# Kernel tuning notes

Measured on AMD Instinct MI355X. Metric: run time of the kernel, lower is better.

## Reference

```python
import jax, jax.numpy as jnp
import numpy as np
from jax import lax

B, P, D = 4, 8192, 512          # 4 point clouds, 8192 pts each, 512-dim features
SCALES = (1.0, 0.5, 0.25)
BIG = 1e10


def fps_indices(pos_b, n_samples):
    """Farthest-point sampling on one cloud. pos_b: [P,3] -> idx [n_samples].
    Deterministic start at index 0 (original uses a random start)."""
    n_pts = pos_b.shape[0]

    def step(carry, _):
        dist, far = carry                       # dist:[P], far: scalar int
        centroid = pos_b[far]                   # [3]
        d = jnp.sum((pos_b - centroid) ** 2, axis=-1)  # [P]
        dist = jnp.minimum(dist, d)
        new_far = jnp.argmax(dist).astype(jnp.int32)
        return (dist, new_far), far

    init = (jnp.full((n_pts,), BIG, dtype=pos_b.dtype), jnp.int32(0))
    _, idx = lax.scan(step, init, None, length=n_samples)
    return idx                                  # [n_samples] int32


def setup_inputs() -> dict:
    key = jax.random.key(0)
    k1, k2 = jax.random.split(key)
    x = jax.random.normal(k1, (B * P, D), dtype=jnp.float32)
    pos = jax.random.normal(k2, (B * P, 3), dtype=jnp.float32)
    batch_idx = jnp.repeat(jnp.arange(B, dtype=jnp.int64), P)  # sorted, equal-sized batches
    return {"x": x, "pos": pos, "batch_idx": batch_idx}


def reference(x, pos, batch_idx):
    # batch_idx is sorted with equal counts -> per-batch view is a reshape
    xb = x.reshape(B, P, D)
    pb = pos.reshape(B, P, 3)

    feats = [xb]          # scale == 1.0 keeps all points
    poss = [pb]
    for s in SCALES[1:]:
        n = max(1, int(P * s))
        idx = jax.vmap(lambda p: fps_indices(p, n))(pb)          # [B, n]
        feats.append(jnp.take_along_axis(xb, idx[:, :, None], axis=1))  # [B, n, D]
        poss.append(jnp.take_along_axis(pb, idx[:, :, None], axis=1))   # [B, n, 3]

    # 'concat' fusion: per-batch concat over scales, then concat over batches
    fused_x = jnp.concatenate(feats, axis=1).reshape(-1, D)
    fused_p = jnp.concatenate(poss, axis=1).reshape(-1, 3)
    return fused_x, fused_p
```

## Files before the change

### kernel.cpp

```cpp
#include <hip/hip_runtime.h>


constexpr int kB   = 4;
constexpr int kP   = 8192;
constexpr int kD   = 512;
constexpr int kN1  = 4096;
constexpr int kN2  = 2048;
constexpr int kS   = kP + kN1 + kN2;
constexpr int kT   = 256;
constexpr int kPts = kP / kT;
constexpr int kG   = 4;
constexpr int kGp  = kPts / kG;

typedef unsigned long long u64;
typedef unsigned u32;

__global__ __launch_bounds__(kT, 1)
void fps_kernel(const float* __restrict__ pos, int* __restrict__ idx_out) {
  const int b    = blockIdx.x;
  const int tid  = threadIdx.x;
  const int wave = tid >> 6;
  const int lane = tid & 63;
  const float* pb = pos + (size_t)b * kP * 3;
  int* idx = idx_out + b * kN1;

  __shared__ __attribute__((aligned(16))) float lds_pos[kP * 3];
  __shared__ u32 lds_key[kP];
  __shared__ float lds_bb[4][6];
  __shared__ u64 lds_wkey[2][4];
  __shared__ float lds_c0[3];

  {
    const float4* src = reinterpret_cast<const float4*>(pb);
    float4* dst = reinterpret_cast<float4*>(lds_pos);
#pragma unroll
    for (int i = 0; i < (kP * 3 / 4) / kT; ++i)
      dst[tid + i * kT] = src[tid + i * kT];
  }
  __syncthreads();

  float mn0 = 1e30f, mn1 = 1e30f, mn2 = 1e30f;
  float mx0 = -1e30f, mx1 = -1e30f, mx2 = -1e30f;
  for (int i = tid; i < kP; i += kT) {
    float x = lds_pos[3 * i], y = lds_pos[3 * i + 1], z = lds_pos[3 * i + 2];
    mn0 = fminf(mn0, x); mx0 = fmaxf(mx0, x);
    mn1 = fminf(mn1, y); mx1 = fmaxf(mx1, y);
    mn2 = fminf(mn2, z); mx2 = fmaxf(mx2, z);
  }
#pragma unroll
  for (int m = 32; m >= 1; m >>= 1) {
    mn0 = fminf(mn0, __shfl_xor(mn0, m, 64)); mx0 = fmaxf(mx0, __shfl_xor(mx0, m, 64));
    mn1 = fminf(mn1, __shfl_xor(mn1, m, 64)); mx1 = fmaxf(mx1, __shfl_xor(mx1, m, 64));
    mn2 = fminf(mn2, __shfl_xor(mn2, m, 64)); mx2 = fmaxf(mx2, __shfl_xor(mx2, m, 64));
  }
  if (lane == 0) {
    lds_bb[wave][0] = mn0; lds_bb[wave][1] = mn1; lds_bb[wave][2] = mn2;
    lds_bb[wave][3] = mx0; lds_bb[wave][4] = mx1; lds_bb[wave][5] = mx2;
  }
  __syncthreads();
#pragma unroll
  for (int w = 0; w < 4; ++w) {
    mn0 = fminf(mn0, lds_bb[w][0]); mn1 = fminf(mn1, lds_bb[w][1]); mn2 = fminf(mn2, lds_bb[w][2]);
    mx0 = fmaxf(mx0, lds_bb[w][3]); mx1 = fmaxf(mx1, lds_bb[w][4]); mx2 = fmaxf(mx2, lds_bb[w][5]);
  }

  {
    const float i0 = 63.0f / fmaxf(mx0 - mn0, 1e-20f);
    const float i1 = 63.0f / fmaxf(mx1 - mn1, 1e-20f);
    const float i2 = 63.0f / fmaxf(mx2 - mn2, 1e-20f);
    for (int i = tid; i < kP; i += kT) {
      int qx = (int)((lds_pos[3 * i]     - mn0) * i0);
      int qy = (int)((lds_pos[3 * i + 1] - mn1) * i1);
      int qz = (int)((lds_pos[3 * i + 2] - mn2) * i2);
      qx = min(max(qx, 0), 63); qy = min(max(qy, 0), 63); qz = min(max(qz, 0), 63);
      u32 code = 0;
#pragma unroll
      for (int t = 0; t < 6; ++t)
        code |= (((u32)(qx >> t) & 1u) << (3 * t)) |
                (((u32)(qy >> t) & 1u) << (3 * t + 1)) |
                (((u32)(qz >> t) & 1u) << (3 * t + 2));
      lds_key[i] = (code << 13) | (u32)i;
    }
  }
  __syncthreads();

  for (int kk = 2; kk <= kP; kk <<= 1) {
    for (int j = kk >> 1; j > 0; j >>= 1) {
      const int mask = j - 1;
#pragma unroll
      for (int it = 0; it < (kP / 2) / kT; ++it) {
        int i = tid + it * kT;
        int a = ((i & ~mask) << 1) | (i & mask);
        int c = a | j;
        u32 x = lds_key[a], y = lds_key[c];
        bool up = ((a & kk) == 0);
        if ((x > y) == up) { lds_key[a] = y; lds_key[c] = x; }
      }
      __syncthreads();
    }
  }

  float px[kPts], py[kPts], pz[kPts], dist_[kPts];
  int lo_[kPts];
  {
    const int base = tid * kPts;
#pragma unroll
    for (int m = 0; m < kPts; ++m) {
      int o = (int)(lds_key[base + m] & 8191u);
      px[m] = lds_pos[3 * o];
      py[m] = lds_pos[3 * o + 1];
      pz[m] = lds_pos[3 * o + 2];
      lo_[m] = 8191 - o;
      dist_[m] = 1e10f;
      if (o == 0) { lds_c0[0] = px[m]; lds_c0[1] = py[m]; lds_c0[2] = pz[m]; }
    }
  }
  __syncthreads();

  {
    const int base3 = tid * kPts * 3;
#pragma unroll
    for (int m = 0; m < kPts; ++m) {
      lds_pos[base3 + 3 * m]     = px[m];
      lds_pos[base3 + 3 * m + 1] = py[m];
      lds_pos[base3 + 3 * m + 2] = pz[m];
    }
  }

  float blx[kG], bhx[kG], bly[kG], bhy[kG], blz[kG], bhz[kG];
  u64 cku[kG];
#pragma unroll
  for (int g = 0; g < kG; ++g) {
    float lx = 1e30f, hx = -1e30f, ly = 1e30f, hy = -1e30f, lz = 1e30f, hz = -1e30f;
    u32 best = 0;
#pragma unroll
    for (int k = 0; k < kGp; ++k) {
      const int m = g * kGp + k;
      lx = fminf(lx, px[m]); hx = fmaxf(hx, px[m]);
      ly = fminf(ly, py[m]); hy = fmaxf(hy, py[m]);
      lz = fminf(lz, pz[m]); hz = fmaxf(hz, pz[m]);
      u32 losp = ((u32)lo_[m] << 13) | (u32)(tid * kPts + m);
      best = best > losp ? best : losp;
    }
    blx[g] = lx; bhx[g] = hx; bly[g] = ly; bhy[g] = hy; blz[g] = lz; bhz[g] = hz;
    cku[g] = ((u64)__float_as_uint(1e10f) << 26) | best;
  }
  __syncthreads();

  float cx = lds_c0[0], cy = lds_c0[1], cz = lds_c0[2];
  int far = 0;
  for (int s = 0; ; ++s) {
    if (tid == 0) idx[s] = far;
    if (s == kN1 - 1) break;

    u64 tk = 0;
#pragma unroll
    for (int g = 0; g < kG; ++g) {
      float gx = fmaxf(fmaxf(blx[g] - cx, cx - bhx[g]), 0.0f);
      float gy = fmaxf(fmaxf(bly[g] - cy, cy - bhy[g]), 0.0f);
      float gz = fmaxf(fmaxf(blz[g] - cz, cz - bhz[g]), 0.0f);
      float lb2 = gx * gx + gy * gy; lb2 = lb2 + gz * gz;
      float cv = __uint_as_float((u32)(cku[g] >> 26));
      if (!(lb2 * 0.999995f >= cv)) {
        float vb = -1.0f; u32 lsb = 0;
        {
#pragma clang fp contract(off)
#pragma unroll
          for (int k = 0; k < kGp; ++k) {
            const int m = g * kGp + k;
            float dx = px[m] - cx;
            float dy = py[m] - cy;
            float dz = pz[m] - cz;
            float d = dx * dx + dy * dy;
            d = d + dz * dz;
            float dk = fminf(dist_[m], d);
            dist_[m] = dk;
            u32 losp = ((u32)lo_[m] << 13) | (u32)(tid * kPts + m);
            bool gt = (dk > vb) || (dk == vb && losp > lsb);
            vb  = gt ? dk : vb;
            lsb = gt ? losp : lsb;
          }
        }
        cku[g] = ((u64)__float_as_uint(vb) << 26) | lsb;
      }
      tk = tk > cku[g] ? tk : cku[g];
    }

#pragma unroll
    for (int m = 32; m >= 1; m >>= 1) {
      u64 o = __shfl_xor(tk, m, 64);
      if (o > tk) tk = o;
    }
    if (lane == 0) lds_wkey[s & 1][wave] = tk;
    __syncthreads();
    u64 k0 = lds_wkey[s & 1][0], k1 = lds_wkey[s & 1][1];
    u64 k2 = lds_wkey[s & 1][2], k3 = lds_wkey[s & 1][3];
    u64 m01 = k0 > k1 ? k0 : k1;
    u64 m23 = k2 > k3 ? k2 : k3;
    u64 mm  = m01 > m23 ? m01 : m23;
    far = 8191 - (int)((mm >> 13) & 0x1FFFu);
    const int sp = (int)(mm & 0x1FFFu);
    cx = lds_pos[3 * sp]; cy = lds_pos[3 * sp + 1]; cz = lds_pos[3 * sp + 2];
  }
}

constexpr int kXRows     = kB * kS;
constexpr int kXBlocks   = kXRows / 2;
constexpr int kPosElems  = kB * kS * 3;
constexpr int kPosBlocks = kPosElems / 256;

__device__ __forceinline__ int src_row(int b, int r, const int* __restrict__ idx) {
  int s;
  if (r < kP)            s = r;
  else if (r < kP + kN1) s = idx[b * kN1 + (r - kP)];
  else                   s = idx[b * kN1 + (r - kP - kN1)];
  return b * kP + s;
}

__global__ __launch_bounds__(256)
void gather_kernel(const float* __restrict__ x, const float* __restrict__ pos,
                   const int* __restrict__ idx, float* __restrict__ out) {
  const int blk = blockIdx.x;
  if (blk < kXBlocks) {
    const int row  = blk * 2 + (threadIdx.x >> 7);
    const int lane = threadIdx.x & 127;
    const int b = row / kS;
    const int r = row - b * kS;
    const int sr = src_row(b, r, idx);
    const float4* src4 = reinterpret_cast<const float4*>(x + (size_t)sr * kD);
    float4* dst4       = reinterpret_cast<float4*>(out + (size_t)row * kD);
    dst4[lane] = src4[lane];
  } else {
    const int e = (blk - kXBlocks) * 256 + threadIdx.x;
    const int row = e / 3;
    const int c   = e - row * 3;
    const int b = row / kS;
    const int r = row - b * kS;
    const int sr = src_row(b, r, idx);
    float* outp = out + (size_t)kB * kS * kD;
    outp[e] = pos[sr * 3 + c];
  }
}

extern "C" void kernel_launch(void* const* d_in, const int* in_sizes, int n_in,
                              void* d_out, int out_size, void* d_ws, size_t ws_size,
                              hipStream_t stream) {
  const float* x   = (const float*)d_in[0];
  const float* pos = (const float*)d_in[1];
  int* idx = (int*)d_ws;

  fps_kernel<<<kB, kT, 0, stream>>>(pos, idx);
  gather_kernel<<<kXBlocks + kPosBlocks, 256, 0, stream>>>(x, pos, idx, (float*)d_out);
}
```

Before: 8.889 ms.

## Reduce FPS argmax with DPP and carry winner coordinates, using 512 threads

The serial farthest-point-sampling loop now uses 512 threads with 2 bounding-box groups per thread instead of 256 threads with 4. The per-wave argmax changes from a 64-bit key reduction using shuffles to DPP row operations. That reduction carries the winning point's distance, tie-break key and xyz coordinates, which removes the dependent LDS lookup of the next centroid and the reordered position write-back. Per-group updates now do the min-distance pass first, then separate max, tie-break and coordinate-select passes. In exchange, the reduction moves five values per stage, the cross-wave merge covers 8 waves instead of 4, and the barrier spans more waves.

Result: faster. 7.537 ms (-15.2%).

```diff
diff --git a/kernel.cpp b/kernel.cpp
--- a/kernel.cpp
+++ b/kernel.cpp
@@ -7,15 +7,38 @@
 constexpr int kN1  = 4096;
 constexpr int kN2  = 2048;
 constexpr int kS   = kP + kN1 + kN2;
-constexpr int kT   = 256;
+constexpr int kT   = 512;
+constexpr int kW   = kT / 64;
 constexpr int kPts = kP / kT;
-constexpr int kG   = 4;
+constexpr int kG   = 2;
 constexpr int kGp  = kPts / kG;
 
 typedef unsigned long long u64;
 typedef unsigned u32;
 
-__global__ __launch_bounds__(kT, 1)
+template <int CTRL>
+__device__ __forceinline__ u32 dpp1(u32 v) {
+  return (u32)__builtin_amdgcn_update_dpp((int)v, (int)v, CTRL, 0xF, 0xF, false);
+}
+
+__device__ __forceinline__ void keymax(float& d, u32& l, u32& x, u32& y, u32& z,
+                                       float od, u32 ol, u32 ox, u32 oy, u32 oz) {
+  bool t = (od > d) || (od == d && ol > l);
+  d = t ? od : d; l = t ? ol : l;
+  x = t ? ox : x; y = t ? oy : y; z = t ? oz : z;
+}
+
+#define DPP_STAGE(CTRL)                                                     \
+  {                                                                         \
+    u32 pd = dpp1<CTRL>(__float_as_uint(kd));                               \
+    u32 pl = dpp1<CTRL>(kl);                                                \
+    u32 qx = dpp1<CTRL>(kx);                                                \
+    u32 qy = dpp1<CTRL>(ky);                                                \
+    u32 qz = dpp1<CTRL>(kz);                                                \
+    keymax(kd, kl, kx, ky, kz, __uint_as_float(pd), pl, qx, qy, qz);        \
+  }
+
+__global__ __launch_bounds__(kT, 2)
 void fps_kernel(const float* __restrict__ pos, int* __restrict__ idx_out) {
   const int b    = blockIdx.x;
   const int tid  = threadIdx.x;
@@ -26,8 +49,8 @@
 
   __shared__ __attribute__((aligned(16))) float lds_pos[kP * 3];
   __shared__ u32 lds_key[kP];
-  __shared__ float lds_bb[4][6];
-  __shared__ u64 lds_wkey[2][4];
+  __shared__ float lds_bb[kW][6];
+  __shared__ __attribute__((aligned(16))) u32 wslot[2][kW][8];
   __shared__ float lds_c0[3];
 
   {
@@ -59,7 +82,7 @@
   }
   __syncthreads();
 #pragma unroll
-  for (int w = 0; w < 4; ++w) {
+  for (int w = 0; w < kW; ++w) {
     mn0 = fminf(mn0, lds_bb[w][0]); mn1 = fminf(mn1, lds_bb[w][1]); mn2 = fminf(mn2, lds_bb[w][2]);
     mx0 = fmaxf(mx0, lds_bb[w][3]); mx1 = fmaxf(mx1, lds_bb[w][4]); mx2 = fmaxf(mx2, lds_bb[w][5]);
   }
@@ -101,7 +124,7 @@
   }
 
   float px[kPts], py[kPts], pz[kPts], dist_[kPts];
-  int lo_[kPts];
+  u32 lo1_[kPts];
   {
     const int base = tid * kPts;
 #pragma unroll
@@ -110,40 +133,32 @@
       px[m] = lds_pos[3 * o];
       py[m] = lds_pos[3 * o + 1];
       pz[m] = lds_pos[3 * o + 2];
-      lo_[m] = 8191 - o;
+      lo1_[m] = (u32)(8192 - o);
       dist_[m] = 1e10f;
       if (o == 0) { lds_c0[0] = px[m]; lds_c0[1] = py[m]; lds_c0[2] = pz[m]; }
     }
   }
-  __syncthreads();
-
-  {
-    const int base3 = tid * kPts * 3;
-#pragma unroll
-    for (int m = 0; m < kPts; ++m) {
-      lds_pos[base3 + 3 * m]     = px[m];
-      lds_pos[base3 + 3 * m + 1] = py[m];
-      lds_pos[base3 + 3 * m + 2] = pz[m];
-    }
-  }
 
   float blx[kG], bhx[kG], bly[kG], bhy[kG], blz[kG], bhz[kG];
-  u64 cku[kG];
+  float cgd[kG]; u32 cgl[kG], cgx[kG], cgy[kG], cgz[kG];
 #pragma unroll
   for (int g = 0; g < kG; ++g) {
     float lx = 1e30f, hx = -1e30f, ly = 1e30f, hy = -1e30f, lz = 1e30f, hz = -1e30f;
-    u32 best = 0;
+    u32 lob = 0, wx = 0, wy = 0, wz = 0;
 #pragma unroll
     for (int k = 0; k < kGp; ++k) {
       const int m = g * kGp + k;
       lx = fminf(lx, px[m]); hx = fmaxf(hx, px[m]);
       ly = fminf(ly, py[m]); hy = fmaxf(hy, py[m]);
       lz = fminf(lz, pz[m]); hz = fmaxf(hz, pz[m]);
-      u32 losp = ((u32)lo_[m] << 13) | (u32)(tid * kPts + m);
-      best = best > losp ? best : losp;
+      bool t = lo1_[m] > lob;
+      lob = t ? lo1_[m] : lob;
+      wx = t ? __float_as_uint(px[m]) : wx;
+      wy = t ? __float_as_uint(py[m]) : wy;
+      wz = t ? __float_as_uint(pz[m]) : wz;
     }
     blx[g] = lx; bhx[g] = hx; bly[g] = ly; bhy[g] = hy; blz[g] = lz; bhz[g] = hz;
-    cku[g] = ((u64)__float_as_uint(1e10f) << 26) | best;
+    cgd[g] = 1e10f; cgl[g] = lob; cgx[g] = wx; cgy[g] = wy; cgz[g] = wz;
   }
   __syncthreads();
 
@@ -153,16 +168,13 @@
     if (tid == 0) idx[s] = far;
     if (s == kN1 - 1) break;
 
-    u64 tk = 0;
 #pragma unroll
     for (int g = 0; g < kG; ++g) {
       float gx = fmaxf(fmaxf(blx[g] - cx, cx - bhx[g]), 0.0f);
       float gy = fmaxf(fmaxf(bly[g] - cy, cy - bhy[g]), 0.0f);
       float gz = fmaxf(fmaxf(blz[g] - cz, cz - bhz[g]), 0.0f);
       float lb2 = gx * gx + gy * gy; lb2 = lb2 + gz * gz;
-      float cv = __uint_as_float((u32)(cku[g] >> 26));
-      if (!(lb2 * 0.999995f >= cv)) {
-        float vb = -1.0f; u32 lsb = 0;
+      if (!(lb2 * 0.999995f >= cgd[g])) {
         {
 #pragma clang fp contract(off)
 #pragma unroll
@@ -173,34 +185,68 @@
             float dz = pz[m] - cz;
             float d = dx * dx + dy * dy;
             d = d + dz * dz;
-            float dk = fminf(dist_[m], d);
-            dist_[m] = dk;
-            u32 losp = ((u32)lo_[m] << 13) | (u32)(tid * kPts + m);
-            bool gt = (dk > vb) || (dk == vb && losp > lsb);
-            vb  = gt ? dk : vb;
-            lsb = gt ? losp : lsb;
+            dist_[m] = fminf(dist_[m], d);
           }
         }
-        cku[g] = ((u64)__float_as_uint(vb) << 26) | lsb;
+        float vb = dist_[g * kGp];
+#pragma unroll
+        for (int k = 1; k < kGp; ++k) vb = fmaxf(vb, dist_[g * kGp + k]);
+        u32 lob = 0;
+#pragma unroll
+        for (int k = 0; k < kGp; ++k) {
+          const int m = g * kGp + k;
+          u32 c = (dist_[m] == vb) ? lo1_[m] : 0u;
+          lob = lob > c ? lob : c;
+        }
+        u32 wx = cgx[g], wy = cgy[g], wz = cgz[g];
+#pragma unroll
+        for (int k = 0; k < kGp; ++k) {
+          const int m = g * kGp + k;
+          bool t = (lo1_[m] == lob);
+          wx = t ? __float_as_uint(px[m]) : wx;
+          wy = t ? __float_as_uint(py[m]) : wy;
+          wz = t ? __float_as_uint(pz[m]) : wz;
+        }
+        cgd[g] = vb; cgl[g] = lob; cgx[g] = wx; cgy[g] = wy; cgz[g] = wz;
       }
-      tk = tk > cku[g] ? tk : cku[g];
-    }
-
-#pragma unroll
-    for (int m = 32; m >= 1; m >>= 1) {
-      u64 o = __shfl_xor(tk, m, 64);
-      if (o > tk) tk = o;
-    }
-    if (lane == 0) lds_wkey[s & 1][wave] = tk;
+    }
+
+    float kd = cgd[0]; u32 kl = cgl[0], kx = cgx[0], ky = cgy[0], kz = cgz[0];
+    keymax(kd, kl, kx, ky, kz, cgd[1], cgl[1], cgx[1], cgy[1], cgz[1]);
+
+    DPP_STAGE(0xB1);
+    DPP_STAGE(0x4E);
+    DPP_STAGE(0x141);
+    DPP_STAGE(0x140);
+    DPP_STAGE(0x142);
+    DPP_STAGE(0x143);
+
+    if (lane == 63) {
+      u32* slot = &wslot[s & 1][wave][0];
+      slot[0] = __float_as_uint(kd); slot[1] = kl;
+      slot[2] = kx; slot[3] = ky; slot[4] = kz;
+    }
     __syncthreads();
-    u64 k0 = lds_wkey[s & 1][0], k1 = lds_wkey[s & 1][1];
-    u64 k2 = lds_wkey[s & 1][2], k3 = lds_wkey[s & 1][3];
-    u64 m01 = k0 > k1 ? k0 : k1;
-    u64 m23 = k2 > k3 ? k2 : k3;
-    u64 mm  = m01 > m23 ? m01 : m23;
-    far = 8191 - (int)((mm >> 13) & 0x1FFFu);
-    const int sp = (int)(mm & 0x1FFFu);
-    cx = lds_pos[3 * sp]; cy = lds_pos[3 * sp + 1]; cz = lds_pos[3 * sp + 2];
+
+    const u32 (*sl)[8] = wslot[s & 1];
+    float sd[kW]; u32 sv[kW], sx[kW], sy[kW], sz[kW];
+#pragma unroll
+    for (int w = 0; w < kW; ++w) {
+      uint4 q = *reinterpret_cast<const uint4*>(&sl[w][0]);
+      sd[w] = __uint_as_float(q.x); sv[w] = q.y;
+      sx[w] = q.z; sy[w] = q.w; sz[w] = sl[w][4];
+    }
+#pragma unroll
+    for (int st = 1; st < kW; st <<= 1)
+#pragma unroll
+      for (int w = 0; w < kW; w += 2 * st)
+        keymax(sd[w], sv[w], sx[w], sy[w], sz[w],
+               sd[w + st], sv[w + st], sx[w + st], sy[w + st], sz[w + st]);
+
+    far = 8192 - (int)sv[0];
+    cx = __uint_as_float(sx[0]);
+    cy = __uint_as_float(sy[0]);
+    cz = __uint_as_float(sz[0]);
   }
 }
 
```
